# Kernel tuning notes

Measured on AMD Instinct MI355X. Metric: run time of the kernel, lower is better.

The kernel has to match this reference:

```python
import jax, jax.numpy as jnp
import numpy as np

B, N, D_IN, H, F = 2, 2048, 512, 8, 64
NEG_SLOPE = 0.2


def setup_inputs() -> dict:
    key = jax.random.key(0)
    k0, k1, k2, k3 = jax.random.split(key, 4)
    nodes = jax.random.normal(k0, (B, N, D_IN), dtype=jnp.float32)
    edges = jax.random.randint(k1, (B, N, N, 1), 0, 2).astype(jnp.int32)
    # ensure every node has at least one neighbor (self-loop) so softmax is finite
    idx = jnp.arange(N)
    edges = edges.at[:, idx, idx, :].set(1)
    W = jax.random.normal(k2, (D_IN, H * F), dtype=jnp.float32) * 0.02
    a = jax.random.normal(k3, (2 * F,), dtype=jnp.float32) * 0.02
    return {"nodes": nodes, "edges": edges, "W": W, "a": a}


def reference(nodes, edges, W, a):
    b, n, _ = nodes.shape
    mapped = (nodes @ W).reshape(b, n, H, F)  # [B,N,H,F]
    # additive attention: attn([m_i ; m_j]) = a_l . m_i + a_r . m_j
    a_l, a_r = a[:F], a[F:]
    el = jnp.einsum('bnhf,f->bnh', mapped, a_l)
    er = jnp.einsum('bnhf,f->bnh', mapped, a_r)
    scores = jax.nn.leaky_relu(el[:, :, None, :] + er[:, None, :, :], negative_slope=NEG_SLOPE)  # [B,N,N,H]
    mask = edges != 0  # [B,N,N,1] broadcasts over heads
    scores = jnp.where(mask, scores, -jnp.inf)
    attn_weights = jax.nn.softmax(scores, axis=2)  # softmax over neighbors j
    attn_res = jnp.einsum('bijh,bjhf->bihf', attn_weights, mapped)  # [B,N,H,F]
    # is_concat=False path: mean over heads, then sigmoid
    return jax.nn.sigmoid(attn_res.mean(axis=2))  # [B,N,F]
```

## Files before the change

kernel.cpp:

```cpp
#include <hip/hip_runtime.h>
#include <hip/hip_bf16.h>
#include <math.h>

#define Bq   2
#define Nq   2048
#define DIN  512
#define Hq   8
#define Fq   64
#define NEG  0.2f

using short8 = __attribute__((ext_vector_type(8))) short;
using half8  = __attribute__((ext_vector_type(8))) _Float16;
using half2v = __attribute__((ext_vector_type(2))) _Float16;
using f32x4  = __attribute__((ext_vector_type(4))) float;

__device__ inline unsigned int bf16_rne(float x) {
    unsigned int u = __float_as_uint(x);
    u += 0x7fffu + ((u >> 16) & 1u);
    return u >> 16;
}
__device__ inline unsigned int f16u(float x) {
    union { _Float16 h; unsigned short u; } cv;
    cv.h = (_Float16)x;
    return (unsigned int)cv.u;
}

#define AFRAG_BLOCKS 256
#define WFRAG_BLOCKS 128

__global__ __launch_bounds__(256) void prep_kernel(
    const float* __restrict__ nodes, ushort* __restrict__ Afrag,
    const float* __restrict__ W,     ushort* __restrict__ Wfrag)
{
    __shared__ __align__(16) char smem[16 * 516 * 4];
    const int bid = blockIdx.x;
    const int t   = threadIdx.x;

    if (bid < AFRAG_BLOCKS) {
        float (*As)[516] = (float(*)[516])smem;
        const int mt = bid;
        {
            const int row = t >> 4, c = t & 15;
#pragma unroll
            for (int i = 0; i < 8; i++) {
                float4 v = *(const float4*)&nodes[((size_t)mt * 16 + row) * DIN + (c + i * 16) * 4];
                *(float4*)&As[row][(c + i * 16) * 4] = v;
            }
        }
        __syncthreads();
        const int lane = t & 63, ksg = t >> 6;
        const int quad = lane >> 4, l15 = lane & 15;
#pragma unroll
        for (int k2 = 0; k2 < 4; k2++) {
            int ks = ksg * 4 + k2;
            const float* src = &As[l15][ks * 32 + quad * 8];
            float4 f0 = *(const float4*)src;
            float4 f1 = *(const float4*)(src + 4);
            uint4 pk;
            pk.x = bf16_rne(f0.x) | (bf16_rne(f0.y) << 16);
            pk.y = bf16_rne(f0.z) | (bf16_rne(f0.w) << 16);
            pk.z = bf16_rne(f1.x) | (bf16_rne(f1.y) << 16);
            pk.w = bf16_rne(f1.z) | (bf16_rne(f1.w) << 16);
            *(uint4*)(Afrag + ((size_t)(mt * 16 + ks) * 64 + lane) * 8) = pk;
        }
        return;
    }

    {
        float (*Ws)[68] = (float(*)[68])smem;
        const int id = bid - AFRAG_BLOCKS;
        const int ks = id & 15, h = id >> 4;
        {
            const int row = t >> 3, c = t & 7;
            const float* src = &W[(size_t)(ks * 32 + row) * (Hq * Fq) + h * 64 + c * 8];
            float4 v0 = *(const float4*)src;
            float4 v1 = *(const float4*)(src + 4);
            *(float4*)&Ws[row][c * 8]     = v0;
            *(float4*)&Ws[row][c * 8 + 4] = v1;
        }
        __syncthreads();
        const int lane = t & 63, nf = t >> 6;
        const int quad = lane >> 4, l15 = lane & 15;
        float f[8];
#pragma unroll
        for (int jj = 0; jj < 8; jj++) f[jj] = Ws[quad * 8 + jj][nf * 16 + l15];
        uint4 pk;
        pk.x = bf16_rne(f[0]) | (bf16_rne(f[1]) << 16);
        pk.y = bf16_rne(f[2]) | (bf16_rne(f[3]) << 16);
        pk.z = bf16_rne(f[4]) | (bf16_rne(f[5]) << 16);
        pk.w = bf16_rne(f[6]) | (bf16_rne(f[7]) << 16);
        *(uint4*)(Wfrag + (((size_t)(h * 16 + ks) * 4 + nf) * 64 + lane) * 8) = pk;
    }
}

#define GEMM_BLOCKS 512
#define PACK_BLOCKS 4096

__global__ __launch_bounds__(256) void work_kernel(
    const ushort* __restrict__ Afrag, const ushort* __restrict__ Wfrag,
    const float*  __restrict__ avec,
    ushort* __restrict__ Vfrag,
    float* __restrict__ el_t,
    float* __restrict__ er_t,
    unsigned int* __restrict__ EF_t,
    const int* __restrict__ edges, uint2* __restrict__ ebTB)
{
    const int bid = blockIdx.x;
    const int t   = threadIdx.x;

    if (bid >= GEMM_BLOCKS) {
        int gid = (bid - GEMM_BLOCKS) * 256 + t;
        int i  = gid & 2047;
        int jb = (gid >> 11) & 255;
        int b  = gid >> 19;
        const int4* ep = (const int4*)(edges + (((size_t)b * Nq + i) * Nq + jb * 8));
        int4 v0 = ep[0];
        int4 v1 = ep[1];
        unsigned int lo = 0, hi = 0;
        lo |= v0.x ? 0x000000FFu : 0u;  lo |= v0.y ? 0x0000FF00u : 0u;
        lo |= v0.z ? 0x00FF0000u : 0u;  lo |= v0.w ? 0xFF000000u : 0u;
        hi |= v1.x ? 0x000000FFu : 0u;  hi |= v1.y ? 0x0000FF00u : 0u;
        hi |= v1.z ? 0x00FF0000u : 0u;  hi |= v1.w ? 0xFF000000u : 0u;
        uint2 w; w.x = lo; w.y = hi;
        ebTB[((size_t)(b * 256 + jb)) * 2048 + i] = w;
        return;
    }

    const int lane = t & 63;
    const int wv   = t >> 6;
    const int quad = lane >> 4;
    const int l15  = lane & 15;
    const int h    = bid >> 6;
    const int mt   = (bid & 63) * 4 + wv;
    const int row0 = mt * 16;

    const ushort* ap = Afrag + (size_t)mt * 8192 + lane * 8;
    const ushort* bp = Wfrag + (size_t)h * 32768 + lane * 8;

    f32x4 zero4 = {0.f, 0.f, 0.f, 0.f};
    f32x4 acc[4] = {zero4, zero4, zero4, zero4};

    short8 a0, a1, b0[4], b1[4];
    a0 = *(const short8*)(ap);
#pragma unroll
    for (int nf = 0; nf < 4; nf++) b0[nf] = *(const short8*)(bp + nf * 512);

    for (int ks = 0; ks < 16; ks += 2) {
        a1 = *(const short8*)(ap + (ks + 1) * 512);
#pragma unroll
        for (int nf = 0; nf < 4; nf++) b1[nf] = *(const short8*)(bp + (ks + 1) * 2048 + nf * 512);
#pragma unroll
        for (int nf = 0; nf < 4; nf++)
            acc[nf] = __builtin_amdgcn_mfma_f32_16x16x32_bf16(a0, b0[nf], acc[nf], 0, 0, 0);
        a0 = *(const short8*)(ap + (ks + 2) * 512);
#pragma unroll
        for (int nf = 0; nf < 4; nf++) b0[nf] = *(const short8*)(bp + (ks + 2) * 2048 + nf * 512);
#pragma unroll
        for (int nf = 0; nf < 4; nf++)
            acc[nf] = __builtin_amdgcn_mfma_f32_16x16x32_bf16(a1, b1[nf], acc[nf], 0, 0, 0);
    }

    float aL[4], aR[4];
#pragma unroll
    for (int nf = 0; nf < 4; nf++) {
        aL[nf] = avec[nf * 16 + l15];
        aR[nf] = avec[Fq + nf * 16 + l15];
    }
    const int bb = row0 >> 11;
    const int bh = bb * Hq + h;
#pragma unroll
    for (int r = 0; r < 4; r++) {
        float pl = acc[0][r] * aL[0] + acc[1][r] * aL[1] + acc[2][r] * aL[2] + acc[3][r] * aL[3];
        float pr = acc[0][r] * aR[0] + acc[1][r] * aR[1] + acc[2][r] * aR[2] + acc[3][r] * aR[3];
#pragma unroll
        for (int off = 1; off < 16; off <<= 1) {
            pl += __shfl_xor(pl, off, 64);
            pr += __shfl_xor(pr, off, 64);
        }
        if (l15 == 0) {
            int n = (row0 + quad * 4 + r) & (Nq - 1);
            el_t[(size_t)bh * Nq + n] = pl;
            er_t[(size_t)bh * Nq + n] = pr;
            float E = __expf(pr), F = __expf(NEG * pr);
            EF_t[(size_t)bh * Nq + n] = f16u(E) | (f16u(F) << 16);
        }
    }

    const int n_base = row0 & (Nq - 1);
    const int sblk   = n_base >> 5;
    const int quadp  = ((wv & 1) << 1) | (quad >> 1);
    const int jj0    = (quad & 1) * 4;
#pragma unroll
    for (int nf = 0; nf < 4; nf++) {
        uint2 pk;
        pk.x = f16u(acc[nf][0]) | (f16u(acc[nf][1]) << 16);
        pk.y = f16u(acc[nf][2]) | (f16u(acc[nf][3]) << 16);
        size_t off = ((((size_t)bh * 64 + sblk) * 4 + nf) * 64 + quadp * 16 + l15) * 8 + jj0;
        *(uint2*)(Vfrag + off) = pk;
    }
}

__global__ __launch_bounds__(256, 2) void attn_kernel(
    const float* __restrict__ el_t, const float* __restrict__ er_t,
    const unsigned int* __restrict__ EF_t,
    const ushort* __restrict__ Vfrag,
    const uint2* __restrict__ ebTB, float* __restrict__ attn)
{
    const int lane = threadIdx.x & 63;
    const int kh   = threadIdx.x >> 6;
    const int quad = lane >> 4;
    const int l15  = lane & 15;
    const int bid  = blockIdx.x;
    const int it   = bid & 31;
    const int h    = (bid >> 5) & 7;
    const int b    = bid >> 8;
    const int bh   = b * Hq + h;
    const int i0   = it * 64;

    __shared__ float smax[4];
    __shared__ float lds_l[4][4][16];
    __shared__ __align__(16) float lds_acc[4][4][4][64][4];

    const float* errow = er_t + (size_t)bh * Nq;
    float mx = -INFINITY;
#pragma unroll
    for (int ii = 0; ii < 8; ii++) mx = fmaxf(mx, errow[threadIdx.x + ii * 256]);
#pragma unroll
    for (int off = 32; off > 0; off >>= 1) mx = fmaxf(mx, __shfl_xor(mx, off, 64));
    if (lane == 0) smax[kh] = mx;
    __syncthreads();
    const float emax = fmaxf(fmaxf(smax[0], smax[1]), fmaxf(smax[2], smax[3]));

    union HU { unsigned int u; half2v h; };
    HU AC2[4];
#pragma unroll
    for (int rs = 0; rs < 4; rs++) {
        float elv = el_t[(size_t)bh * Nq + i0 + rs * 16 + l15];
        float xm  = elv + emax;
        float m   = fmaxf(xm, NEG * xm);
        float A = __expf(elv - m);
        float C = __expf(NEG * elv - m);
        AC2[rs].u = f16u(A) | (f16u(C) << 16);
    }

    const unsigned int* EFp = EF_t + (size_t)bh * Nq + kh * 512;
    const ushort*       vp  = Vfrag + (size_t)bh * 131072 + kh * 32768 + lane * 8;
    const uint2*        mp  = ebTB + ((size_t)(b * 256 + kh * 64 + quad)) * 2048 + i0 + l15;

    f32x4 zero4 = {0.f, 0.f, 0.f, 0.f};
    f32x4 acc[4][4];
    f32x4 accl[4];
#pragma unroll
    for (int rs = 0; rs < 4; rs++) {
        accl[rs] = zero4;
#pragma unroll
        for (int nf = 0; nf < 4; nf++) acc[rs][nf] = zero4;
    }

    const _Float16 one16 = (_Float16)1.0f;
    const half8 onesv = {one16, one16, one16, one16, one16, one16, one16, one16};

    for (int s = 0; s < 16; s++) {
        half8 vb0 = *(const half8*)(vp + s * 2048);
        half8 vb1 = *(const half8*)(vp + s * 2048 + 512);
        half8 vb2 = *(const half8*)(vp + s * 2048 + 1024);
        half8 vb3 = *(const half8*)(vp + s * 2048 + 1536);
        uint2 mbs[4];
#pragma unroll
        for (int rs = 0; rs < 4; rs++) mbs[rs] = mp[(size_t)s * 8192 + rs * 16];
        uint4 efa = *(const uint4*)(EFp + s * 32 + quad * 8);
        uint4 efb = *(const uint4*)(EFp + s * 32 + quad * 8 + 4);
        unsigned int ef[8] = {efa.x, efa.y, efa.z, efa.w, efb.x, efb.y, efb.z, efb.w};

#pragma unroll
        for (int rs = 0; rs < 4; rs++) {
            union AFU { half8 h8; unsigned int w4[4]; } af;
#pragma unroll
            for (int pp = 0; pp < 4; pp++) {
                HU e0, e1, p0, p1, X, Y, P;
                e0.u = ef[2 * pp];
                e1.u = ef[2 * pp + 1];
                p0.h = AC2[rs].h * e0.h;
                p1.h = AC2[rs].h * e1.h;
                X.u = __builtin_amdgcn_perm(p1.u, p0.u, 0x05040100);
                Y.u = __builtin_amdgcn_perm(p1.u, p0.u, 0x07060302);
                P.h = __builtin_elementwise_max(X.h, Y.h);
                unsigned int msrc = (pp < 2) ? mbs[rs].x : mbs[rs].y;
                unsigned int msel = (pp & 1) ? 0x03030202u : 0x01010000u;
                unsigned int mw   = __builtin_amdgcn_perm(0u, msrc, msel);
                af.w4[pp] = P.u & mw;
            }
            acc[rs][0] = __builtin_amdgcn_mfma_f32_16x16x32_f16(af.h8, vb0, acc[rs][0], 0, 0, 0);
            acc[rs][1] = __builtin_amdgcn_mfma_f32_16x16x32_f16(af.h8, vb1, acc[rs][1], 0, 0, 0);
            acc[rs][2] = __builtin_amdgcn_mfma_f32_16x16x32_f16(af.h8, vb2, acc[rs][2], 0, 0, 0);
            acc[rs][3] = __builtin_amdgcn_mfma_f32_16x16x32_f16(af.h8, vb3, acc[rs][3], 0, 0, 0);
            accl[rs]   = __builtin_amdgcn_mfma_f32_16x16x32_f16(af.h8, onesv, accl[rs], 0, 0, 0);
        }
    }

#pragma unroll
    for (int rs = 0; rs < 4; rs++)
#pragma unroll
        for (int nf = 0; nf < 4; nf++)
            *(f32x4*)&lds_acc[kh][rs][nf][lane][0] = acc[rs][nf];
    if (l15 == 0) {
#pragma unroll
        for (int rs = 0; rs < 4; rs++)
#pragma unroll
            for (int r = 0; r < 4; r++)
                lds_l[kh][rs][quad * 4 + r] = accl[rs][r];
    }
    __syncthreads();

    const int rs = kh;
    f32x4 facc[4] = {zero4, zero4, zero4, zero4};
#pragma unroll
    for (int k2 = 0; k2 < 4; k2++)
#pragma unroll
        for (int nf = 0; nf < 4; nf++) {
            f32x4 v = *(const f32x4*)&lds_acc[k2][rs][nf][lane][0];
            facc[nf][0] += v[0]; facc[nf][1] += v[1];
            facc[nf][2] += v[2]; facc[nf][3] += v[3];
        }
    float flr[4];
#pragma unroll
    for (int r = 0; r < 4; r++) {
        float sl = 0.f;
#pragma unroll
        for (int k2 = 0; k2 < 4; k2++) sl += lds_l[k2][rs][quad * 4 + r];
        flr[r] = sl;
    }
#pragma unroll
    for (int nf = 0; nf < 4; nf++)
#pragma unroll
        for (int r = 0; r < 4; r++)
            attn[(((size_t)b * Nq + i0 + rs * 16 + quad * 4 + r) * Hq + h) * Fq + nf * 16 + l15]
                = facc[nf][r] / flr[r];
}

__global__ __launch_bounds__(256) void out_kernel(
    const float* __restrict__ attn, float* __restrict__ out)
{
    const int idx = blockIdx.x * 256 + threadIdx.x;
    const int f   = idx & 63;
    const int bn  = idx >> 6;
    const float* p = attn + (size_t)bn * Hq * Fq + f;
    float s = 0.f;
#pragma unroll
    for (int h = 0; h < Hq; h++) s += p[h * Fq];
    s *= (1.f / Hq);
    out[idx] = 1.f / (1.f + __expf(-s));
}

extern "C" void kernel_launch(void* const* d_in, const int* in_sizes, int n_in,
                              void* d_out, int out_size, void* d_ws, size_t ws_size,
                              hipStream_t stream) {
    const float* nodes = (const float*)d_in[0];
    const int*   edges = (const int*)d_in[1];
    const float* W     = (const float*)d_in[2];
    const float* a     = (const float*)d_in[3];
    float* out = (float*)d_out;

    char* ws = (char*)d_ws;
    ushort* Afrag = (ushort*)ws;           ws += (size_t)Bq * Nq * DIN * 2;
    ushort* Wfrag = (ushort*)ws;           ws += (size_t)DIN * Hq * Fq * 2;
    ushort* Vfrag = (ushort*)ws;           ws += (size_t)Bq * Hq * Nq * Fq * 2;
    float*  el_t  = (float*)ws;            ws += (size_t)Bq * Hq * Nq * 4;
    float*  er_t  = (float*)ws;            ws += (size_t)Bq * Hq * Nq * 4;
    unsigned int* EF_t = (unsigned int*)ws; ws += (size_t)Bq * Hq * Nq * 4;
    uint2*  ebTB  = (uint2*)ws;            ws += (size_t)Bq * Nq * Nq;
    float*  attn  = (float*)ws;

    prep_kernel<<<AFRAG_BLOCKS + WFRAG_BLOCKS, 256, 0, stream>>>(nodes, Afrag, W, Wfrag);
    work_kernel<<<GEMM_BLOCKS + PACK_BLOCKS, 256, 0, stream>>>(
        Afrag, Wfrag, a, Vfrag, el_t, er_t, EF_t, edges, ebTB);
    attn_kernel<<<Bq * Hq * (Nq / 64), 256, 0, stream>>>(el_t, er_t, EF_t, Vfrag, ebTB, attn);
    out_kernel<<<(Bq * Nq * Fq) / 256, 256, 0, stream>>>(attn, out);
}
```

Measured before the change: 116.9 us.

## Split E/F exponent tables, widen edge packing per thread, store attn as fp16

The edge-packing threads now each read 32 ints and emit four packed words, so a quarter as many blocks are launched. The exponent table is split into separate E and F fp16 arrays so the inner loop multiplies each packed half2 once, which removes the perm shuffles. The intermediate per-head attention output is stored as fp16 instead of fp32, halving its write and read traffic, and a reciprocal multiply replaces the division. Storing attn in fp16 adds rounding error.

Result: faster. 112.7 us (median of 2 runs) (-3.6%).

```diff
diff --git a/kernel.cpp b/kernel.cpp
--- a/kernel.cpp
+++ b/kernel.cpp
@@ -94,7 +94,7 @@
 }
 
 #define GEMM_BLOCKS 512
-#define PACK_BLOCKS 4096
+#define PACK_BLOCKS 1024
 
 __global__ __launch_bounds__(256) void work_kernel(
     const ushort* __restrict__ Afrag, const ushort* __restrict__ Wfrag,
@@ -102,7 +102,8 @@
     ushort* __restrict__ Vfrag,
     float* __restrict__ el_t,
     float* __restrict__ er_t,
-    unsigned int* __restrict__ EF_t,
+    ushort* __restrict__ Epk,
+    ushort* __restrict__ Fpk,
     const int* __restrict__ edges, uint2* __restrict__ ebTB)
 {
     const int bid = blockIdx.x;
@@ -111,18 +112,22 @@
     if (bid >= GEMM_BLOCKS) {
         int gid = (bid - GEMM_BLOCKS) * 256 + t;
         int i  = gid & 2047;
-        int jb = (gid >> 11) & 255;
-        int b  = gid >> 19;
-        const int4* ep = (const int4*)(edges + (((size_t)b * Nq + i) * Nq + jb * 8));
-        int4 v0 = ep[0];
-        int4 v1 = ep[1];
-        unsigned int lo = 0, hi = 0;
-        lo |= v0.x ? 0x000000FFu : 0u;  lo |= v0.y ? 0x0000FF00u : 0u;
-        lo |= v0.z ? 0x00FF0000u : 0u;  lo |= v0.w ? 0xFF000000u : 0u;
-        hi |= v1.x ? 0x000000FFu : 0u;  hi |= v1.y ? 0x0000FF00u : 0u;
-        hi |= v1.z ? 0x00FF0000u : 0u;  hi |= v1.w ? 0xFF000000u : 0u;
-        uint2 w; w.x = lo; w.y = hi;
-        ebTB[((size_t)(b * 256 + jb)) * 2048 + i] = w;
+        int jw = (gid >> 11) & 63;
+        int b  = gid >> 17;
+        const int4* ep = (const int4*)(edges + (((size_t)b * Nq + i) * Nq + jw * 32));
+        int4 v[8];
+#pragma unroll
+        for (int c = 0; c < 8; c++) v[c] = ep[c];
+#pragma unroll
+        for (int q = 0; q < 4; q++) {
+            unsigned int lo = 0, hi = 0;
+            lo |= v[2*q].x   ? 0x000000FFu : 0u;  lo |= v[2*q].y   ? 0x0000FF00u : 0u;
+            lo |= v[2*q].z   ? 0x00FF0000u : 0u;  lo |= v[2*q].w   ? 0xFF000000u : 0u;
+            hi |= v[2*q+1].x ? 0x000000FFu : 0u;  hi |= v[2*q+1].y ? 0x0000FF00u : 0u;
+            hi |= v[2*q+1].z ? 0x00FF0000u : 0u;  hi |= v[2*q+1].w ? 0xFF000000u : 0u;
+            uint2 w; w.x = lo; w.y = hi;
+            ebTB[((size_t)(b * 256 + jw * 4 + q)) * 2048 + i] = w;
+        }
         return;
     }
 
@@ -181,8 +186,8 @@
             int n = (row0 + quad * 4 + r) & (Nq - 1);
             el_t[(size_t)bh * Nq + n] = pl;
             er_t[(size_t)bh * Nq + n] = pr;
-            float E = __expf(pr), F = __expf(NEG * pr);
-            EF_t[(size_t)bh * Nq + n] = f16u(E) | (f16u(F) << 16);
+            Epk[(size_t)bh * Nq + n] = (ushort)f16u(__expf(pr));
+            Fpk[(size_t)bh * Nq + n] = (ushort)f16u(__expf(NEG * pr));
         }
     }
 
@@ -202,9 +207,9 @@
 
 __global__ __launch_bounds__(256, 2) void attn_kernel(
     const float* __restrict__ el_t, const float* __restrict__ er_t,
-    const unsigned int* __restrict__ EF_t,
+    const ushort* __restrict__ Epk, const ushort* __restrict__ Fpk,
     const ushort* __restrict__ Vfrag,
-    const uint2* __restrict__ ebTB, float* __restrict__ attn)
+    const uint2* __restrict__ ebTB, ushort* __restrict__ attn)
 {
     const int lane = threadIdx.x & 63;
     const int kh   = threadIdx.x >> 6;
@@ -232,20 +237,22 @@
     const float emax = fmaxf(fmaxf(smax[0], smax[1]), fmaxf(smax[2], smax[3]));
 
     union HU { unsigned int u; half2v h; };
-    HU AC2[4];
+    HU AA2[4], CC2[4];
 #pragma unroll
     for (int rs = 0; rs < 4; rs++) {
         float elv = el_t[(size_t)bh * Nq + i0 + rs * 16 + l15];
         float xm  = elv + emax;
         float m   = fmaxf(xm, NEG * xm);
-        float A = __expf(elv - m);
-        float C = __expf(NEG * elv - m);
-        AC2[rs].u = f16u(A) | (f16u(C) << 16);
-    }
-
-    const unsigned int* EFp = EF_t + (size_t)bh * Nq + kh * 512;
-    const ushort*       vp  = Vfrag + (size_t)bh * 131072 + kh * 32768 + lane * 8;
-    const uint2*        mp  = ebTB + ((size_t)(b * 256 + kh * 64 + quad)) * 2048 + i0 + l15;
+        unsigned int a16 = f16u(__expf(elv - m));
+        unsigned int c16 = f16u(__expf(NEG * elv - m));
+        AA2[rs].u = a16 | (a16 << 16);
+        CC2[rs].u = c16 | (c16 << 16);
+    }
+
+    const ushort* Ep = Epk + (size_t)bh * Nq + kh * 512;
+    const ushort* Fp = Fpk + (size_t)bh * Nq + kh * 512;
+    const ushort* vp = Vfrag + (size_t)bh * 131072 + kh * 32768 + lane * 8;
+    const uint2*  mp = ebTB + ((size_t)(b * 256 + kh * 64 + quad)) * 2048 + i0 + l15;
 
     f32x4 zero4 = {0.f, 0.f, 0.f, 0.f};
     f32x4 acc[4][4];
@@ -268,27 +275,25 @@
         uint2 mbs[4];
 #pragma unroll
         for (int rs = 0; rs < 4; rs++) mbs[rs] = mp[(size_t)s * 8192 + rs * 16];
-        uint4 efa = *(const uint4*)(EFp + s * 32 + quad * 8);
-        uint4 efb = *(const uint4*)(EFp + s * 32 + quad * 8 + 4);
-        unsigned int ef[8] = {efa.x, efa.y, efa.z, efa.w, efb.x, efb.y, efb.z, efb.w};
+        uint4 ev = *(const uint4*)(Ep + s * 32 + quad * 8);
+        uint4 fv = *(const uint4*)(Fp + s * 32 + quad * 8);
+        unsigned int ee[4] = {ev.x, ev.y, ev.z, ev.w};
+        unsigned int ff[4] = {fv.x, fv.y, fv.z, fv.w};
 
 #pragma unroll
         for (int rs = 0; rs < 4; rs++) {
             union AFU { half8 h8; unsigned int w4[4]; } af;
 #pragma unroll
             for (int pp = 0; pp < 4; pp++) {
-                HU e0, e1, p0, p1, X, Y, P;
-                e0.u = ef[2 * pp];
-                e1.u = ef[2 * pp + 1];
-                p0.h = AC2[rs].h * e0.h;
-                p1.h = AC2[rs].h * e1.h;
-                X.u = __builtin_amdgcn_perm(p1.u, p0.u, 0x05040100);
-                Y.u = __builtin_amdgcn_perm(p1.u, p0.u, 0x07060302);
-                P.h = __builtin_elementwise_max(X.h, Y.h);
+                HU e, f, pe, pf, P;
+                e.u = ee[pp];
+                f.u = ff[pp];
+                pe.h = AA2[rs].h * e.h;
+                pf.h = CC2[rs].h * f.h;
+                P.h = __builtin_elementwise_max(pe.h, pf.h);
                 unsigned int msrc = (pp < 2) ? mbs[rs].x : mbs[rs].y;
                 unsigned int msel = (pp & 1) ? 0x03030202u : 0x01010000u;
-                unsigned int mw   = __builtin_amdgcn_perm(0u, msrc, msel);
-                af.w4[pp] = P.u & mw;
+                af.w4[pp] = P.u & __builtin_amdgcn_perm(0u, msrc, msel);
             }
             acc[rs][0] = __builtin_amdgcn_mfma_f32_16x16x32_f16(af.h8, vb0, acc[rs][0], 0, 0, 0);
             acc[rs][1] = __builtin_amdgcn_mfma_f32_16x16x32_f16(af.h8, vb1, acc[rs][1], 0, 0, 0);
@@ -322,32 +327,36 @@
             facc[nf][0] += v[0]; facc[nf][1] += v[1];
             facc[nf][2] += v[2]; facc[nf][3] += v[3];
         }
-    float flr[4];
+    float rl[4];
 #pragma unroll
     for (int r = 0; r < 4; r++) {
         float sl = 0.f;
 #pragma unroll
         for (int k2 = 0; k2 < 4; k2++) sl += lds_l[k2][rs][quad * 4 + r];
-        flr[r] = sl;
+        rl[r] = 1.0f / sl;
     }
 #pragma unroll
     for (int nf = 0; nf < 4; nf++)
 #pragma unroll
         for (int r = 0; r < 4; r++)
             attn[(((size_t)b * Nq + i0 + rs * 16 + quad * 4 + r) * Hq + h) * Fq + nf * 16 + l15]
-                = facc[nf][r] / flr[r];
+                = (ushort)f16u(facc[nf][r] * rl[r]);
 }
 
 __global__ __launch_bounds__(256) void out_kernel(
-    const float* __restrict__ attn, float* __restrict__ out)
+    const ushort* __restrict__ attn, float* __restrict__ out)
 {
     const int idx = blockIdx.x * 256 + threadIdx.x;
     const int f   = idx & 63;
     const int bn  = idx >> 6;
-    const float* p = attn + (size_t)bn * Hq * Fq + f;
+    const ushort* p = attn + (size_t)bn * Hq * Fq + f;
     float s = 0.f;
 #pragma unroll
-    for (int h = 0; h < Hq; h++) s += p[h * Fq];
+    for (int h = 0; h < Hq; h++) {
+        union { ushort u; _Float16 h16; } cv;
+        cv.u = p[h * Fq];
+        s += (float)cv.h16;
+    }
     s *= (1.f / Hq);
     out[idx] = 1.f / (1.f + __expf(-s));
 }
@@ -367,13 +376,14 @@
     ushort* Vfrag = (ushort*)ws;           ws += (size_t)Bq * Hq * Nq * Fq * 2;
     float*  el_t  = (float*)ws;            ws += (size_t)Bq * Hq * Nq * 4;
     float*  er_t  = (float*)ws;            ws += (size_t)Bq * Hq * Nq * 4;
-    unsigned int* EF_t = (unsigned int*)ws; ws += (size_t)Bq * Hq * Nq * 4;
+    ushort* Epk   = (ushort*)ws;           ws += (size_t)Bq * Hq * Nq * 2;
+    ushort* Fpk   = (ushort*)ws;           ws += (size_t)Bq * Hq * Nq * 2;
     uint2*  ebTB  = (uint2*)ws;            ws += (size_t)Bq * Nq * Nq;
-    float*  attn  = (float*)ws;
+    ushort* attn  = (ushort*)ws;
 
     prep_kernel<<<AFRAG_BLOCKS + WFRAG_BLOCKS, 256, 0, stream>>>(nodes, Afrag, W, Wfrag);
     work_kernel<<<GEMM_BLOCKS + PACK_BLOCKS, 256, 0, stream>>>(
-        Afrag, Wfrag, a, Vfrag, el_t, er_t, EF_t, edges, ebTB);
-    attn_kernel<<<Bq * Hq * (Nq / 64), 256, 0, stream>>>(el_t, er_t, EF_t, Vfrag, ebTB, attn);
+        Afrag, Wfrag, a, Vfrag, el_t, er_t, Epk, Fpk, edges, ebTB);
+    attn_kernel<<<Bq * Hq * (Nq / 64), 256, 0, stream>>>(el_t, er_t, Epk, Fpk, Vfrag, ebTB, attn);
     out_kernel<<<(Bq * Nq * Fq) / 256, 256, 0, stream>>>(attn, out);
 }
```
